# Optimization experiments

Measured on AMD Instinct MI355X. Metric: run time of the kernel, lower is better.

## Reference

```python
import jax, jax.numpy as jnp
import numpy as np

N = 100_000        # nodes
E = 1_600_000      # edges
G = 256            # graphs in batch
C_IN = 128
NUM_CLASSES = 10


def _rn(k, shape, s=0.1):
    return jax.random.normal(k, shape, jnp.float32) * s


def setup_inputs() -> dict:
    key = jax.random.key(0)
    ks = jax.random.split(key, 32)
    inp = {
        "x": jax.random.normal(ks[0], (N, C_IN), jnp.float32),
        "edge_index": jax.random.randint(ks[1], (2, E), 0, N, jnp.int64) if jax.config.jax_enable_x64 else jax.random.randint(ks[1], (2, E), 0, N, jnp.int32),
        "batch": jnp.sort(jax.random.randint(ks[2], (N,), 0, G)),
        "tolerance": jax.random.normal(ks[3], (1, 1), jnp.float32),
        "cost": jax.random.normal(ks[4], (1, 1), jnp.float32),
        "time": jax.random.normal(ks[5], (1, 1), jnp.float32),
        "quantity": jax.random.normal(ks[6], (1, 1), jnp.float32),
        # GCNConv weights (x @ W then aggregate, + bias)
        "W1": _rn(ks[7], (C_IN, 64)), "b1": _rn(ks[8], (64,)),
        "W2": _rn(ks[9], (64, 16)), "b2": _rn(ks[10], (16,)),
        # residual projections
        "Wr1": _rn(ks[11], (C_IN, 64)), "br1": _rn(ks[12], (64,)),
        "Wr2": _rn(ks[13], (64, 16)), "br2": _rn(ks[14], (16,)),
        "alpha1": jnp.float32(0.5), "alpha2": jnp.float32(0.5),
        # 4 metrics MLPs stacked: Linear(1,8) -> SiLU -> Linear(8,16)
        "mW1": _rn(ks[15], (4, 1, 8)), "mb1": _rn(ks[16], (4, 8)),
        "mW2": _rn(ks[17], (4, 8, 16)), "mb2": _rn(ks[18], (4, 16)),
        # classifier head
        "Wf1": _rn(ks[19], (80, 80)), "bf1": _rn(ks[20], (80,)),
        "Wf2": _rn(ks[21], (80, NUM_CLASSES)), "bf2": _rn(ks[22], (NUM_CLASSES,)),
    }
    return inp


def _gcn_norm(src, dst, n):
    # add self loops, symmetric normalization: norm_e = d^-1/2[src] * d^-1/2[dst]
    loop = jnp.arange(n, dtype=src.dtype)
    src2 = jnp.concatenate([src, loop])
    dst2 = jnp.concatenate([dst, loop])
    deg = jax.ops.segment_sum(jnp.ones_like(dst2, jnp.float32), dst2, num_segments=n)
    dinv = jnp.where(deg > 0, jax.lax.rsqrt(jnp.maximum(deg, 1.0)), 0.0)
    norm = dinv[src2] * dinv[dst2]
    return src2, dst2, norm


def _gcn_conv(x, W, b, src2, dst2, norm, n):
    h = x @ W                                 # [N, out]
    msg = h[src2] * norm[:, None]             # gather + scale  [E+N, out]
    return jax.ops.segment_sum(msg, dst2, num_segments=n) + b


def reference(x, edge_index, batch, tolerance, cost, time, quantity,
              W1, b1, W2, b2, Wr1, br1, Wr2, br2, alpha1, alpha2,
              mW1, mb1, mW2, mb2, Wf1, bf1, Wf2, bf2):
    silu = jax.nn.silu
    n = x.shape[0]
    src2, dst2, norm = _gcn_norm(edge_index[0], edge_index[1], n)

    # encoder
    r1 = silu(x @ Wr1 + br1)
    h = silu(_gcn_conv(x, W1, b1, src2, dst2, norm, n))
    h = h + r1 * alpha1
    r2 = silu(h @ Wr2 + br2)
    z = _gcn_conv(h, W2, b2, src2, dst2, norm, n)
    z = z + r2 * alpha2                       # [N, 16]

    # global mean pool over graphs
    sums = jax.ops.segment_sum(z, batch, num_segments=G)
    cnts = jax.ops.segment_sum(jnp.ones((n,), z.dtype), batch, num_segments=G)
    graph_emb = sums / jnp.maximum(cnts, 1.0)[:, None]   # [G, 16]

    # metrics embedding: 4 tiny MLPs, stacked  m:[4,1,1]
    m = jnp.stack([tolerance, cost, time, quantity])
    e = silu(jnp.einsum('gij,gjk->gik', m, mW1) + mb1[:, None, :])
    e = jnp.einsum('gij,gjk->gik', e, mW2) + mb2[:, None, :]   # [4,1,16]
    metrics = jnp.tile(e.transpose(1, 0, 2).reshape(1, 64), (G, 1))  # [G,64]

    combined = jnp.concatenate([graph_emb, metrics], axis=1)  # [G, 80]
    out = silu(combined @ Wf1 + bf1)
    return out @ Wf2 + bf2                                    # [G, num_classes]
```

## Files before the change

kernel.cpp:

```cpp
#include <hip/hip_runtime.h>

static __device__ __forceinline__ float silu_f(float v) {
    return v / (1.0f + __expf(-v));
}
static __device__ __forceinline__ unsigned short f2bf(float f) {
    unsigned int u = __float_as_uint(f);
    u = (u + 0x7FFFu + ((u >> 16) & 1u)) >> 16;
    return (unsigned short)u;
}
static __device__ __forceinline__ float bf2f(unsigned short h) {
    return __uint_as_float(((unsigned int)h) << 16);
}


extern "C" __global__ __launch_bounds__(256) void k_bhist(
    const int* __restrict__ dst, int* __restrict__ bcount, int E, int nbkt, int shift)
{
    __shared__ int lh[512];
    int t = threadIdx.x;
    for (int i = t; i < 512; i += 256) lh[i] = 0;
    __syncthreads();
    int e0 = blockIdx.x * 8192;
    #pragma unroll 4
    for (int i = 0; i < 32; i++) {
        int e = e0 + t + i * 256;
        if (e < E) atomicAdd(&lh[dst[e] >> shift], 1);
    }
    __syncthreads();
    for (int b = t; b < nbkt; b += 256)
        if (lh[b]) atomicAdd(&bcount[b], lh[b]);
}

extern "C" __global__ __launch_bounds__(512) void k_bscan(
    const int* __restrict__ bcount, int* __restrict__ boff, int* __restrict__ bcursor, int nbkt)
{
    __shared__ int sc[512];
    int t = threadIdx.x;
    int v = (t < nbkt) ? bcount[t] : 0;
    sc[t] = v;
    __syncthreads();
    for (int off = 1; off < 512; off <<= 1) {
        int add = (t >= off) ? sc[t - off] : 0;
        __syncthreads();
        sc[t] += add;
        __syncthreads();
    }
    int excl = sc[t] - v;
    if (t < nbkt) { boff[t] = excl; bcursor[t] = excl; }
    if (t == nbkt - 1) boff[nbkt] = excl + v;
}

extern "C" __global__ __launch_bounds__(256) void k_bscatter(
    const int* __restrict__ src, const int* __restrict__ dst, int* __restrict__ bcursor,
    int2* __restrict__ ebuf, int E, int nbkt, int shift)
{
    __shared__ int lh[512];
    __shared__ int lbase[512];
    int t = threadIdx.x;
    for (int i = t; i < 512; i += 256) lh[i] = 0;
    __syncthreads();
    int e0 = blockIdx.x * 8192;
    #pragma unroll 4
    for (int i = 0; i < 32; i++) {
        int e = e0 + t + i * 256;
        if (e < E) atomicAdd(&lh[dst[e] >> shift], 1);
    }
    __syncthreads();
    for (int b = t; b < nbkt; b += 256)
        lbase[b] = lh[b] ? atomicAdd(&bcursor[b], lh[b]) : 0;
    __syncthreads();
    #pragma unroll 4
    for (int i = 0; i < 32; i++) {
        int e = e0 + t + i * 256;
        if (e < E) {
            int d = dst[e];
            int p = atomicAdd(&lbase[d >> shift], 1);
            ebuf[p] = make_int2(src[e], d);
        }
    }
}

extern "C" __global__ __launch_bounds__(256) void k_bdeg_scan(
    const int2* __restrict__ ebuf, const int* __restrict__ boff,
    int* __restrict__ deg, float* __restrict__ dinv, int* __restrict__ rowstart,
    int shift, int N)
{
    int b = blockIdx.x;
    int W = 1 << shift;
    __shared__ int lcur[4096];
    __shared__ int sc[256];
    int t = threadIdx.x;
    for (int i = t; i < W; i += 256) lcur[i] = 0;
    __syncthreads();
    int s = boff[b], e_ = boff[b + 1];
    for (int e = s + t; e < e_; e += 256)
        atomicAdd(&lcur[ebuf[e].y - (b << shift)], 1);
    __syncthreads();

    int c = W >> 8;
    int base = t * c;
    int mysum = 0;
    for (int i = 0; i < c; i++) mysum += lcur[base + i];
    sc[t] = mysum;
    __syncthreads();
    int mine = mysum;
    for (int off = 1; off < 256; off <<= 1) {
        int add = (t >= off) ? sc[t - off] : 0;
        __syncthreads();
        sc[t] += add;
        __syncthreads();
    }
    int run = sc[t] - mine + s;
    int nbase = b << shift;
    for (int i = 0; i < c; i++) {
        int d = lcur[base + i];
        int node = nbase + base + i;
        if (node < N) {
            rowstart[node] = run;
            deg[node] = d;
            dinv[node] = rsqrtf((float)(d + 1));
        }
        run += d;
    }
}

extern "C" __global__ __launch_bounds__(256) void k_bfill(
    const int2* __restrict__ ebuf, const int* __restrict__ boff,
    const int* __restrict__ rowstart, int* __restrict__ csr, int shift)
{
    int b = blockIdx.x;
    int W = 1 << shift;
    __shared__ int lcur[4096];
    int t = threadIdx.x;
    for (int i = t; i < W; i += 256) lcur[i] = 0;
    __syncthreads();
    int s = boff[b], e_ = boff[b + 1];
    for (int e = s + t; e < e_; e += 256) {
        int2 p = ebuf[e];
        int pos = atomicAdd(&lcur[p.y - (b << shift)], 1);
        csr[rowstart[p.y] + pos] = p.x;
    }
}

extern "C" __global__ __launch_bounds__(512) void k_gemm1(
    const float* __restrict__ x, const float* __restrict__ W1, const float* __restrict__ Wr1,
    const float* __restrict__ br1, const float* __restrict__ dinv,
    unsigned short* __restrict__ h0s, float* __restrict__ r1, int n)
{
    __shared__ float xs[128 * 36];
    int t = threadIdx.x;
    int lane = t & 63;
    int wv = __builtin_amdgcn_readfirstlane(t >> 6);
    const float* Wp = (wv < 4) ? W1 : Wr1;
    const int c0 = (wv & 3) * 16;
    int r0 = blockIdx.x * 128;

    float acc0[16] = {}, acc1[16] = {};
    float4 px[2];

    #pragma unroll
    for (int i = 0; i < 2; i++) {
        int u = t + i * 512;
        int rr = u >> 3, kq = u & 7;
        px[i] = make_float4(0.f, 0.f, 0.f, 0.f);
        if (r0 + rr < n) px[i] = *(const float4*)&x[(size_t)(r0 + rr) * 128 + kq * 4];
    }

    for (int kk = 0; kk < 128; kk += 32) {
        if (kk) __syncthreads();
        #pragma unroll
        for (int i = 0; i < 2; i++) {
            int u = t + i * 512;
            int rr = u >> 3, kq = u & 7;
            *(float4*)&xs[rr * 36 + kq * 4] = px[i];
        }
        __syncthreads();
        if (kk < 96) {
            int kn = kk + 32;
            #pragma unroll
            for (int i = 0; i < 2; i++) {
                int u = t + i * 512;
                int rr = u >> 3, kq = u & 7;
                px[i] = make_float4(0.f, 0.f, 0.f, 0.f);
                if (r0 + rr < n) px[i] = *(const float4*)&x[(size_t)(r0 + rr) * 128 + kn + kq * 4];
            }
        }
        #pragma unroll
        for (int kb = 0; kb < 8; kb++) {
            float4 xa = *(const float4*)&xs[lane * 36 + kb * 4];
            float4 xb = *(const float4*)&xs[(lane + 64) * 36 + kb * 4];
            float xv0[4] = {xa.x, xa.y, xa.z, xa.w};
            float xv1[4] = {xb.x, xb.y, xb.z, xb.w};
            #pragma unroll
            for (int kq = 0; kq < 4; kq++) {
                const float* wrow = &Wp[(size_t)(kk + kb * 4 + kq) * 64 + c0];
                #pragma unroll
                for (int j = 0; j < 4; j++) {
                    float4 w4 = *(const float4*)&wrow[j * 4];
                    acc0[j*4+0] += xv0[kq] * w4.x; acc1[j*4+0] += xv1[kq] * w4.x;
                    acc0[j*4+1] += xv0[kq] * w4.y; acc1[j*4+1] += xv1[kq] * w4.y;
                    acc0[j*4+2] += xv0[kq] * w4.z; acc1[j*4+2] += xv1[kq] * w4.z;
                    acc0[j*4+3] += xv0[kq] * w4.w; acc1[j*4+3] += xv1[kq] * w4.w;
                }
            }
        }
    }

    #pragma unroll
    for (int half = 0; half < 2; half++) {
        int row = r0 + half * 64 + lane;
        if (row >= n) continue;
        const float* a = half ? acc1 : acc0;
        if (wv < 4) {
            float dv = dinv[row];
            uint4 o0, o1;
            unsigned int* po = &o0.x;
            #pragma unroll
            for (int q = 0; q < 8; q++) {
                unsigned int lo = f2bf(a[q*2+0] * dv);
                unsigned int hi = f2bf(a[q*2+1] * dv);
                po[q] = lo | (hi << 16);
            }
            uint4* dst0 = (uint4*)&h0s[(size_t)row * 64 + c0];
            dst0[0] = o0; dst0[1] = o1;
        } else {
            #pragma unroll
            for (int j = 0; j < 4; j++) {
                float4 b = *(const float4*)&br1[c0 + j * 4];
                float4 o = make_float4(silu_f(a[j*4+0]+b.x), silu_f(a[j*4+1]+b.y),
                                       silu_f(a[j*4+2]+b.z), silu_f(a[j*4+3]+b.w));
                *(float4*)&r1[(size_t)row * 64 + c0 + j * 4] = o;
            }
        }
    }
}

extern "C" __global__ __launch_bounds__(256) void k_agg1(
    const unsigned short* __restrict__ h0s, const int* __restrict__ rowstart,
    const int* __restrict__ deg, const int* __restrict__ csr,
    const float* __restrict__ dinv, const float* __restrict__ b1,
    const float* __restrict__ alpha1, float* __restrict__ r1h, int n)
{
    int wave = threadIdx.x >> 6, lane = threadIdx.x & 63;
    int node = blockIdx.x * 4 + wave;
    if (node >= n) return;
    int rs = rowstart[node];
    int cnt = deg[node];
    float acc = bf2f(h0s[(size_t)node * 64 + lane]);
    int i = 0;
    for (; i + 8 <= cnt; i += 8) {
        int s0 = csr[rs+i+0], s1 = csr[rs+i+1], s2 = csr[rs+i+2], s3 = csr[rs+i+3];
        int s4 = csr[rs+i+4], s5 = csr[rs+i+5], s6 = csr[rs+i+6], s7 = csr[rs+i+7];
        float a0 = bf2f(h0s[(size_t)s0*64+lane]), a1 = bf2f(h0s[(size_t)s1*64+lane]);
        float a2 = bf2f(h0s[(size_t)s2*64+lane]), a3 = bf2f(h0s[(size_t)s3*64+lane]);
        float a4 = bf2f(h0s[(size_t)s4*64+lane]), a5 = bf2f(h0s[(size_t)s5*64+lane]);
        float a6 = bf2f(h0s[(size_t)s6*64+lane]), a7 = bf2f(h0s[(size_t)s7*64+lane]);
        acc += ((a0+a1)+(a2+a3)) + ((a4+a5)+(a6+a7));
    }
    for (; i < cnt; i++) acc += bf2f(h0s[(size_t)csr[rs+i]*64+lane]);
    float v = dinv[node] * acc + b1[lane];
    float hv = silu_f(v) + r1h[(size_t)node * 64 + lane] * alpha1[0];
    r1h[(size_t)node * 64 + lane] = hv;
}

extern "C" __global__ __launch_bounds__(256) void k_gemm2(
    const float* __restrict__ h, const float* __restrict__ W2, const float* __restrict__ Wr2,
    const float* __restrict__ br2, const float* __restrict__ dinv,
    float* __restrict__ h2s, float* __restrict__ r2, int n)
{
    __shared__ float xsT[64 * 132];
    __shared__ float wsm[64 * 32];
    int t = threadIdx.x;
    int r0 = blockIdx.x * 128;
    int rg = t >> 3;
    int cg = t & 7;
    float acc[4][4] = {};

    #pragma unroll
    for (int i = 0; i < 8; i++) {
        int u = t + i * 256;
        int row = u >> 4, kq = u & 15;
        float4 v = make_float4(0.f, 0.f, 0.f, 0.f);
        int grow = r0 + row;
        if (grow < n) v = *(const float4*)&h[(size_t)grow * 64 + kq * 4];
        xsT[(kq * 4 + 0) * 132 + row] = v.x;
        xsT[(kq * 4 + 1) * 132 + row] = v.y;
        xsT[(kq * 4 + 2) * 132 + row] = v.z;
        xsT[(kq * 4 + 3) * 132 + row] = v.w;
    }
    #pragma unroll
    for (int i = 0; i < 2; i++) {
        int ul = t + i * 256;
        int k = ul >> 3, u = ul & 7;
        int c = u * 4;
        float4 v;
        if (c < 16) v = *(const float4*)&W2[(size_t)k * 16 + c];
        else        v = *(const float4*)&Wr2[(size_t)k * 16 + (c - 16)];
        *(float4*)&wsm[k * 32 + c] = v;
    }
    __syncthreads();

    const float* xbase = &xsT[rg * 4];
    const float* wbase = &wsm[cg * 4];
    #pragma unroll
    for (int k = 0; k < 64; k++) {
        float4 xa = *(const float4*)&xbase[k * 132];
        float4 wa = *(const float4*)&wbase[k * 32];
        float xv[4] = {xa.x, xa.y, xa.z, xa.w};
        float wv[4] = {wa.x, wa.y, wa.z, wa.w};
        #pragma unroll
        for (int i = 0; i < 4; i++)
            #pragma unroll
            for (int j = 0; j < 4; j++) acc[i][j] += xv[i] * wv[j];
    }

    if (cg < 4) {
        int c0 = cg * 4;
        #pragma unroll
        for (int i = 0; i < 4; i++) {
            int row = r0 + rg * 4 + i;
            if (row >= n) break;
            float dv = dinv[row];
            float4 o = make_float4(acc[i][0]*dv, acc[i][1]*dv, acc[i][2]*dv, acc[i][3]*dv);
            *(float4*)&h2s[(size_t)row * 16 + c0] = o;
        }
    } else {
        int c0 = (cg - 4) * 4;
        float4 b = *(const float4*)&br2[c0];
        #pragma unroll
        for (int i = 0; i < 4; i++) {
            int row = r0 + rg * 4 + i;
            if (row >= n) break;
            float4 o = make_float4(silu_f(acc[i][0]+b.x), silu_f(acc[i][1]+b.y),
                                   silu_f(acc[i][2]+b.z), silu_f(acc[i][3]+b.w));
            *(float4*)&r2[(size_t)row * 16 + c0] = o;
        }
    }
}

extern "C" __global__ __launch_bounds__(256) void k_agg2(
    const float* __restrict__ h2s, const int* __restrict__ rowstart, const int* __restrict__ deg,
    const int* __restrict__ csr, const float* __restrict__ dinv, const float* __restrict__ b2,
    const float* __restrict__ alpha2, float* __restrict__ r2z, int n)
{
    int wave = threadIdx.x >> 6, lane = threadIdx.x & 63;
    int node = blockIdx.x * 4 + wave;
    if (node >= n) return;
    int rs = rowstart[node], cnt = deg[node];
    int sub = lane >> 4, j = lane & 15;
    float acc = 0.0f;
    int i = sub;
    for (; i + 8 <= cnt; i += 8) {
        int sa = csr[rs + i], sb = csr[rs + i + 4];
        acc += h2s[(size_t)sa * 16 + j] + h2s[(size_t)sb * 16 + j];
    }
    for (; i < cnt; i += 4) acc += h2s[(size_t)csr[rs + i] * 16 + j];
    acc += __shfl_xor(acc, 16, 64);
    acc += __shfl_xor(acc, 32, 64);
    if (sub == 0) {
        acc += h2s[(size_t)node * 16 + j];
        float v = dinv[node] * acc + b2[j] + r2z[(size_t)node * 16 + j] * alpha2[0];
        r2z[(size_t)node * 16 + j] = v;
    }
}

extern "C" __global__ __launch_bounds__(256) void k_poolhead(
    const float* __restrict__ z, const int* __restrict__ batch,
    const float* __restrict__ tol, const float* __restrict__ cost,
    const float* __restrict__ time_, const float* __restrict__ qty,
    const float* __restrict__ mW1, const float* __restrict__ mb1,
    const float* __restrict__ mW2, const float* __restrict__ mb2,
    const float* __restrict__ Wf1, const float* __restrict__ bf1,
    const float* __restrict__ Wf2, const float* __restrict__ bf2,
    float* __restrict__ out, int n, int NC)
{
    int g = blockIdx.x;
    __shared__ float comb[80];
    __shared__ float part[16][17];
    __shared__ float hidden[80];
    int t = threadIdx.x;

    int lo = 0, hi = n;
    while (lo < hi) { int m = (lo + hi) >> 1; if (batch[m] < g) lo = m + 1; else hi = m; }
    int start = lo;
    lo = start; hi = n;
    while (lo < hi) { int m = (lo + hi) >> 1; if (batch[m] < g + 1) lo = m + 1; else hi = m; }
    int end = lo;

    int j = t & 15, grp = t >> 4;
    float acc = 0.0f;
    for (int r = start + grp; r < end; r += 16) acc += z[(size_t)r * 16 + j];
    part[grp][j] = acc;
    __syncthreads();
    if (t < 16) {
        float s = 0.0f;
        #pragma unroll
        for (int q = 0; q < 16; q++) s += part[q][t];
        comb[t] = s / fmaxf((float)(end - start), 1.0f);
    } else if (t >= 64 && t < 128) {
        int tt = t - 64;
        int i = tt >> 4, jj = tt & 15;
        float mv = (i == 0) ? tol[0] : (i == 1) ? cost[0] : (i == 2) ? time_[0] : qty[0];
        float a = mb2[i * 16 + jj];
        #pragma unroll
        for (int k = 0; k < 8; k++) {
            float hpre = mv * mW1[i * 8 + k] + mb1[i * 8 + k];
            a += silu_f(hpre) * mW2[i * 128 + k * 16 + jj];
        }
        comb[16 + tt] = a;
    }
    __syncthreads();
    if (t < 80) {
        float a = bf1[t];
        #pragma unroll 8
        for (int k = 0; k < 80; k++) a += comb[k] * Wf1[k * 80 + t];
        hidden[t] = silu_f(a);
    }
    __syncthreads();
    if (t < NC) {
        float a = bf2[t];
        #pragma unroll 8
        for (int k = 0; k < 80; k++) a += hidden[k] * Wf2[k * NC + t];
        out[g * NC + t] = a;
    }
}

extern "C" void kernel_launch(void* const* d_in, const int* in_sizes, int n_in,
                              void* d_out, int out_size, void* d_ws, size_t ws_size,
                              hipStream_t stream)
{
    const float* x     = (const float*)d_in[0];
    const int*   ei    = (const int*)d_in[1];
    const int*   batch = (const int*)d_in[2];
    const float* tol   = (const float*)d_in[3];
    const float* cost  = (const float*)d_in[4];
    const float* time_ = (const float*)d_in[5];
    const float* qty   = (const float*)d_in[6];
    const float* W1    = (const float*)d_in[7];
    const float* b1    = (const float*)d_in[8];
    const float* W2    = (const float*)d_in[9];
    const float* b2    = (const float*)d_in[10];
    const float* Wr1   = (const float*)d_in[11];
    const float* br1   = (const float*)d_in[12];
    const float* Wr2   = (const float*)d_in[13];
    const float* br2   = (const float*)d_in[14];
    const float* alpha1= (const float*)d_in[15];
    const float* alpha2= (const float*)d_in[16];
    const float* mW1   = (const float*)d_in[17];
    const float* mb1   = (const float*)d_in[18];
    const float* mW2   = (const float*)d_in[19];
    const float* mb2   = (const float*)d_in[20];
    const float* Wf1   = (const float*)d_in[21];
    const float* bf1   = (const float*)d_in[22];
    const float* Wf2   = (const float*)d_in[23];
    const float* bf2   = (const float*)d_in[24];

    const int N  = in_sizes[2];
    const int E  = in_sizes[1] / 2;
    const int NC = in_sizes[24];
    const int G  = out_size / NC;

    const int* srcIdx = ei;
    const int* dstIdx = ei + E;

    int shift = 8;
    while (((N + (1 << shift) - 1) >> shift) > 512) shift++;
    const int nbkt = (N + (1 << shift) - 1) >> shift;

    char* w = (char*)d_ws;
    auto alloc = [&](size_t bytes) { char* p = w; w += (bytes + 255) & ~(size_t)255; return p; };
    int*   deg      = (int*)alloc((size_t)N * 4);
    int*   rowstart = (int*)alloc((size_t)N * 4);
    int*   bcount   = (int*)alloc(2048);
    int*   boff     = (int*)alloc(2052 + 252);
    int*   bcursor  = (int*)alloc(2048);
    int*   csr      = (int*)alloc((size_t)E * 4);
    int2*  ebuf     = (int2*)alloc((size_t)E * 8);
    float* dinv     = (float*)alloc((size_t)N * 4);
    unsigned short* h0sb = (unsigned short*)alloc((size_t)N * 64 * 2);
    float* bufA     = (float*)alloc((size_t)N * 64 * 4);
    float* bufB     = (float*)alloc((size_t)N * 64 * 4);
    float* bufC     = (float*)alloc((size_t)N * 16 * 4);

    hipMemsetAsync(bcount, 0, 2048, stream);

    int EB8 = (E + 8191) / 8192;

    k_bhist    <<<EB8, 256, 0, stream>>>(dstIdx, bcount, E, nbkt, shift);
    k_bscan    <<<1, 512, 0, stream>>>(bcount, boff, bcursor, nbkt);
    k_bscatter <<<EB8, 256, 0, stream>>>(srcIdx, dstIdx, bcursor, ebuf, E, nbkt, shift);
    k_bdeg_scan<<<nbkt, 256, 0, stream>>>(ebuf, boff, deg, dinv, rowstart, shift, N);
    k_bfill    <<<nbkt, 256, 0, stream>>>(ebuf, boff, rowstart, csr, shift);

    k_gemm1<<<(N + 127) / 128, 512, 0, stream>>>(x, W1, Wr1, br1, dinv, h0sb, bufB, N);
    k_agg1 <<<(N + 3) / 4, 256, 0, stream>>>(h0sb, rowstart, deg, csr, dinv, b1, alpha1, bufB, N);
    k_gemm2<<<(N + 127) / 128, 256, 0, stream>>>(bufB, W2, Wr2, br2, dinv, bufA, bufC, N);
    k_agg2 <<<(N + 3) / 4, 256, 0, stream>>>(bufA, rowstart, deg, csr, dinv, b2, alpha2, bufC, N);
    k_poolhead<<<G, 256, 0, stream>>>(bufC, batch, tol, cost, time_, qty,
                                      mW1, mb1, mW2, mb2, Wf1, bf1, Wf2, bf2,
                                      (float*)d_out, N, NC);
}
```

Baseline: 273.4 us.

## Fuse CSR degree-scan and fill kernels; widen gemm1 row tile to 256

Merges the per-bucket degree/scan kernel with the CSR fill kernel. The scanned running offsets are kept in shared memory and used directly as atomic cursors, which removes one launch, a second pass over the edge buffer and the rowstart gather. Separately, gemm1 now processes 256 rows per block with four accumulator sets, so each weight load from global/L1 is reused across more rows. The wider tile doubles the shared-memory tile and register use, which may lower occupancy, and with about 391 blocks the GPU may be less evenly filled.

Result: slower. 287.1 us (+5.0%).

```diff
diff --git a/kernel.cpp b/kernel.cpp
--- a/kernel.cpp
+++ b/kernel.cpp
@@ -80,10 +80,10 @@
     }
 }
 
-extern "C" __global__ __launch_bounds__(256) void k_bdeg_scan(
+extern "C" __global__ __launch_bounds__(256) void k_bcsr(
     const int2* __restrict__ ebuf, const int* __restrict__ boff,
     int* __restrict__ deg, float* __restrict__ dinv, int* __restrict__ rowstart,
-    int shift, int N)
+    int* __restrict__ csr, int shift, int N)
 {
     int b = blockIdx.x;
     int W = 1 << shift;
@@ -120,25 +120,14 @@
             deg[node] = d;
             dinv[node] = rsqrtf((float)(d + 1));
         }
+        lcur[base + i] = run;
         run += d;
     }
-}
-
-extern "C" __global__ __launch_bounds__(256) void k_bfill(
-    const int2* __restrict__ ebuf, const int* __restrict__ boff,
-    const int* __restrict__ rowstart, int* __restrict__ csr, int shift)
-{
-    int b = blockIdx.x;
-    int W = 1 << shift;
-    __shared__ int lcur[4096];
-    int t = threadIdx.x;
-    for (int i = t; i < W; i += 256) lcur[i] = 0;
-    __syncthreads();
-    int s = boff[b], e_ = boff[b + 1];
+    __syncthreads();
     for (int e = s + t; e < e_; e += 256) {
         int2 p = ebuf[e];
         int pos = atomicAdd(&lcur[p.y - (b << shift)], 1);
-        csr[rowstart[p.y] + pos] = p.x;
+        csr[pos] = p.x;
     }
 }
 
@@ -147,19 +136,19 @@
     const float* __restrict__ br1, const float* __restrict__ dinv,
     unsigned short* __restrict__ h0s, float* __restrict__ r1, int n)
 {
-    __shared__ float xs[128 * 36];
+    __shared__ float xs[256 * 36];
     int t = threadIdx.x;
     int lane = t & 63;
     int wv = __builtin_amdgcn_readfirstlane(t >> 6);
     const float* Wp = (wv < 4) ? W1 : Wr1;
     const int c0 = (wv & 3) * 16;
-    int r0 = blockIdx.x * 128;
-
-    float acc0[16] = {}, acc1[16] = {};
-    float4 px[2];
+    int r0 = blockIdx.x * 256;
+
+    float acc0[16] = {}, acc1[16] = {}, acc2[16] = {}, acc3[16] = {};
+    float4 px[4];
 
     #pragma unroll
-    for (int i = 0; i < 2; i++) {
+    for (int i = 0; i < 4; i++) {
         int u = t + i * 512;
         int rr = u >> 3, kq = u & 7;
         px[i] = make_float4(0.f, 0.f, 0.f, 0.f);
@@ -169,7 +158,7 @@
     for (int kk = 0; kk < 128; kk += 32) {
         if (kk) __syncthreads();
         #pragma unroll
-        for (int i = 0; i < 2; i++) {
+        for (int i = 0; i < 4; i++) {
             int u = t + i * 512;
             int rr = u >> 3, kq = u & 7;
             *(float4*)&xs[rr * 36 + kq * 4] = px[i];
@@ -178,7 +167,7 @@
         if (kk < 96) {
             int kn = kk + 32;
             #pragma unroll
-            for (int i = 0; i < 2; i++) {
+            for (int i = 0; i < 4; i++) {
                 int u = t + i * 512;
                 int rr = u >> 3, kq = u & 7;
                 px[i] = make_float4(0.f, 0.f, 0.f, 0.f);
@@ -187,10 +176,14 @@
         }
         #pragma unroll
         for (int kb = 0; kb < 8; kb++) {
-            float4 xa = *(const float4*)&xs[lane * 36 + kb * 4];
-            float4 xb = *(const float4*)&xs[(lane + 64) * 36 + kb * 4];
-            float xv0[4] = {xa.x, xa.y, xa.z, xa.w};
-            float xv1[4] = {xb.x, xb.y, xb.z, xb.w};
+            float4 fa = *(const float4*)&xs[lane * 36 + kb * 4];
+            float4 fb = *(const float4*)&xs[(lane + 64) * 36 + kb * 4];
+            float4 fc = *(const float4*)&xs[(lane + 128) * 36 + kb * 4];
+            float4 fd = *(const float4*)&xs[(lane + 192) * 36 + kb * 4];
+            float xv0[4] = {fa.x, fa.y, fa.z, fa.w};
+            float xv1[4] = {fb.x, fb.y, fb.z, fb.w};
+            float xv2[4] = {fc.x, fc.y, fc.z, fc.w};
+            float xv3[4] = {fd.x, fd.y, fd.z, fd.w};
             #pragma unroll
             for (int kq = 0; kq < 4; kq++) {
                 const float* wrow = &Wp[(size_t)(kk + kb * 4 + kq) * 64 + c0];
@@ -198,19 +191,23 @@
                 for (int j = 0; j < 4; j++) {
                     float4 w4 = *(const float4*)&wrow[j * 4];
                     acc0[j*4+0] += xv0[kq] * w4.x; acc1[j*4+0] += xv1[kq] * w4.x;
+                    acc2[j*4+0] += xv2[kq] * w4.x; acc3[j*4+0] += xv3[kq] * w4.x;
                     acc0[j*4+1] += xv0[kq] * w4.y; acc1[j*4+1] += xv1[kq] * w4.y;
+                    acc2[j*4+1] += xv2[kq] * w4.y; acc3[j*4+1] += xv3[kq] * w4.y;
                     acc0[j*4+2] += xv0[kq] * w4.z; acc1[j*4+2] += xv1[kq] * w4.z;
+                    acc2[j*4+2] += xv2[kq] * w4.z; acc3[j*4+2] += xv3[kq] * w4.z;
                     acc0[j*4+3] += xv0[kq] * w4.w; acc1[j*4+3] += xv1[kq] * w4.w;
+                    acc2[j*4+3] += xv2[kq] * w4.w; acc3[j*4+3] += xv3[kq] * w4.w;
                 }
             }
         }
     }
 
     #pragma unroll
-    for (int half = 0; half < 2; half++) {
-        int row = r0 + half * 64 + lane;
+    for (int r = 0; r < 4; r++) {
+        int row = r0 + r * 64 + lane;
         if (row >= n) continue;
-        const float* a = half ? acc1 : acc0;
+        const float* a = (r == 0) ? acc0 : (r == 1) ? acc1 : (r == 2) ? acc2 : acc3;
         if (wv < 4) {
             float dv = dinv[row];
             uint4 o0, o1;
@@ -486,13 +483,12 @@
 
     int EB8 = (E + 8191) / 8192;
 
-    k_bhist    <<<EB8, 256, 0, stream>>>(dstIdx, bcount, E, nbkt, shift);
-    k_bscan    <<<1, 512, 0, stream>>>(bcount, boff, bcursor, nbkt);
-    k_bscatter <<<EB8, 256, 0, stream>>>(srcIdx, dstIdx, bcursor, ebuf, E, nbkt, shift);
-    k_bdeg_scan<<<nbkt, 256, 0, stream>>>(ebuf, boff, deg, dinv, rowstart, shift, N);
-    k_bfill    <<<nbkt, 256, 0, stream>>>(ebuf, boff, rowstart, csr, shift);
-
-    k_gemm1<<<(N + 127) / 128, 512, 0, stream>>>(x, W1, Wr1, br1, dinv, h0sb, bufB, N);
+    k_bhist   <<<EB8, 256, 0, stream>>>(dstIdx, bcount, E, nbkt, shift);
+    k_bscan   <<<1, 512, 0, stream>>>(bcount, boff, bcursor, nbkt);
+    k_bscatter<<<EB8, 256, 0, stream>>>(srcIdx, dstIdx, bcursor, ebuf, E, nbkt, shift);
+    k_bcsr    <<<nbkt, 256, 0, stream>>>(ebuf, boff, deg, dinv, rowstart, csr, shift, N);
+
+    k_gemm1<<<(N + 255) / 256, 512, 0, stream>>>(x, W1, Wr1, br1, dinv, h0sb, bufB, N);
     k_agg1 <<<(N + 3) / 4, 256, 0, stream>>>(h0sb, rowstart, deg, csr, dinv, b1, alpha1, bufB, N);
     k_gemm2<<<(N + 127) / 128, 256, 0, stream>>>(bufB, W2, Wr2, br2, dinv, bufA, bufC, N);
     k_agg2 <<<(N + 3) / 4, 256, 0, stream>>>(bufA, rowstart, deg, csr, dinv, b2, alpha2, bufC, N);
```
